# Optimization experiments

Measured on AMD Instinct MI355X. Metric: run time of the kernel, lower is better.

The kernel has to match this reference:

```python
import jax, jax.numpy as jnp
import numpy as np

N = 50000
V = 3
DIM = 128
H = 64


def setup_inputs() -> dict:
    key = jax.random.key(0)
    ks = jax.random.split(key, 8)
    x = jax.random.normal(ks[0], (N, V * DIM), dtype=jnp.float32)
    edge_index = jax.random.randint(ks[1], (2, 800000), 0, N, dtype=jnp.int64)
    Wv = jax.random.normal(ks[2], (V, DIM, H), dtype=jnp.float32) * (1.0 / np.sqrt(DIM))
    bv = jnp.zeros((V, H), dtype=jnp.float32)
    na_w = jax.random.normal(ks[3], (H, 1), dtype=jnp.float32) * (1.0 / np.sqrt(H))
    na_b = jnp.zeros((1,), dtype=jnp.float32)
    va_w1 = jax.random.normal(ks[4], (H, H // 2), dtype=jnp.float32) * (1.0 / np.sqrt(H))
    va_b1 = jnp.zeros((H // 2,), dtype=jnp.float32)
    va_w2 = jax.random.normal(ks[5], (H // 2, 1), dtype=jnp.float32) * (1.0 / np.sqrt(H // 2))
    va_b2 = jnp.zeros((1,), dtype=jnp.float32)
    cls_w = jax.random.normal(ks[6], (H, 2), dtype=jnp.float32) * (1.0 / np.sqrt(H))
    cls_b = jnp.zeros((2,), dtype=jnp.float32)
    return dict(x=x, edge_index=edge_index, Wv=Wv, bv=bv, na_w=na_w, na_b=na_b,
                va_w1=va_w1, va_b1=va_b1, va_w2=va_w2, va_b2=va_b2,
                cls_w=cls_w, cls_b=cls_b)


def reference(x, edge_index, Wv, bv, na_w, na_b, va_w1, va_b1, va_w2, va_b2, cls_w, cls_b):
    n = x.shape[0]
    # split into equal-dim views: [N, V, DIM]
    xv = x.reshape(n, V, DIM)

    # --- GCNConv (PyG defaults): linear transform, add self-loops, sym-norm aggregate, bias ---
    h = jnp.einsum('nvd,vdh->nvh', xv, Wv)  # [N, V, H]

    src = edge_index[0]
    dst = edge_index[1]
    loop = jnp.arange(n, dtype=src.dtype)
    src_full = jnp.concatenate([src, loop])
    dst_full = jnp.concatenate([dst, loop])

    ones = jnp.ones(src_full.shape[0], dtype=h.dtype)
    deg = jax.ops.segment_sum(ones, dst_full, num_segments=n)  # in-degree incl. self-loop
    dinv = jnp.where(deg > 0, 1.0 / jnp.sqrt(deg), 0.0)
    norm = dinv[src_full] * dinv[dst_full]  # [E+N]

    msgs = h[src_full] * norm[:, None, None]            # [E+N, V, H]
    agg = jax.ops.segment_sum(msgs, dst_full, num_segments=n)  # [N, V, H]
    agg = agg + bv[None, :, :]

    # ReLU
    emb = jax.nn.relu(agg)  # [N, V, H]

    # --- NodeAttentionLayer: softmax over nodes (dim=0), applied per view ---
    scores = jnp.einsum('nvh,ho->nvo', emb, na_w) + na_b  # [N, V, 1]
    att = jax.nn.softmax(scores, axis=0)
    emb_w = emb * att  # [N, V, H]

    # --- ViewAttention ---
    avg = jnp.mean(emb_w, axis=0)  # [V, H]
    vs = jnp.tanh(avg @ va_w1 + va_b1) @ va_w2 + va_b2  # [V, 1]
    vw = jax.nn.softmax(vs.T, axis=1)  # [1, V]
    fused = jnp.einsum('nvh,v->nh', emb_w, vw[0])  # [N, H]

    # --- classifier + log_softmax ---
    logits = fused @ cls_w + cls_b
    logp = jax.nn.log_softmax(logits, axis=1)
    return logp, fused, vw[0]
```

## Files before the change

### kernel.cpp

```cpp
#include <hip/hip_runtime.h>
#include <math.h>

#define NV 3
#define DIMX 128
#define HD 64
#define NVH 192
#define NBLK 256
#define NBUK 128
#define BSH 9

typedef unsigned int uint32;
typedef unsigned short ushort16;
typedef __attribute__((ext_vector_type(8))) short short8;
typedef __attribute__((ext_vector_type(4))) float f32x4;

__device__ __forceinline__ unsigned fkey(float f){
  unsigned b = __float_as_uint(f);
  return (b & 0x80000000u) ? ~b : (b | 0x80000000u);
}
__device__ __forceinline__ float unkey(unsigned k){
  return __uint_as_float((k & 0x80000000u) ? (k ^ 0x80000000u) : ~k);
}
__device__ __forceinline__ uint32 bf16rne(float f){
  uint32 u = __float_as_uint(f);
  return (u + 0x7fffu + ((u >> 16) & 1u)) >> 16;
}
__device__ __forceinline__ float bflo(uint32 p){ return __uint_as_float(p << 16); }
__device__ __forceinline__ float bfhi(uint32 p){ return __uint_as_float(p & 0xffff0000u); }
__device__ __forceinline__ float bfus(uint32 q){ return __uint_as_float(q << 16); }

__global__ __launch_bounds__(256) void k_hist(const int* __restrict__ ei, int E, int EPB,
                                              int* __restrict__ histT){
  __shared__ int sh[NBUK];
  int t = threadIdx.x, b = blockIdx.x;
  if (t < NBUK) sh[t] = 0;
  __syncthreads();
  int e0 = b*EPB, e1 = min(e0 + EPB, E);
  for (int i = e0 + t; i < e1; i += 256){
    int d = ei[E + i];
    atomicAdd(&sh[d >> BSH], 1);
  }
  __syncthreads();
  if (t < NBUK) histT[t*NBLK + b] = sh[t];
}

__global__ __launch_bounds__(1024) void k_hscan(int* __restrict__ histT){
  __shared__ int sh[1024];
  int t = threadIdx.x;
  int lo = t*32;
  int vals[32]; int s = 0;
  #pragma unroll
  for (int k = 0; k < 32; ++k){ vals[k] = histT[lo+k]; s += vals[k]; }
  sh[t] = s; __syncthreads();
  for (int ofs = 1; ofs < 1024; ofs <<= 1){
    int v = (t >= ofs) ? sh[t-ofs] : 0;
    __syncthreads();
    sh[t] += v;
    __syncthreads();
  }
  int run = sh[t] - s;
  #pragma unroll
  for (int k = 0; k < 32; ++k){ histT[lo+k] = run; run += vals[k]; }
}

__global__ __launch_bounds__(256) void k_scatter(const int* __restrict__ ei, int E, int EPB,
                                                 const int* __restrict__ ofsT, int2* __restrict__ ebuf){
  __shared__ int cur[NBUK];
  int t = threadIdx.x, b = blockIdx.x;
  if (t < NBUK) cur[t] = ofsT[t*NBLK + b];
  __syncthreads();
  int e0 = b*EPB, e1 = min(e0 + EPB, E);
  for (int i = e0 + t; i < e1; i += 256){
    int s = ei[i], d = ei[E + i];
    int pos = atomicAdd(&cur[d >> BSH], 1);
    ebuf[pos] = make_int2(s, d);
  }
}

__global__ __launch_bounds__(512) void k_csr(const int2* __restrict__ ebuf, const int* __restrict__ ofsT,
                                             int E, int N, int* __restrict__ rowstart,
                                             float* __restrict__ dinv, int* __restrict__ csr){
  __shared__ int cnt[512];
  __shared__ int pre[512];
  int t = threadIdx.x, b = blockIdx.x;
  int estart = ofsT[b*NBLK];
  int eend   = ((b+1)*NBLK < NBUK*NBLK) ? ofsT[(b+1)*NBLK] : E;
  int n0 = b << BSH;
  int nn = min(512, N - n0);
  cnt[t] = 0;
  __syncthreads();
  for (int i = estart + t; i < eend; i += 512){
    int d = ebuf[i].y;
    atomicAdd(&cnt[d - n0], 1);
  }
  __syncthreads();
  int c = cnt[t];
  pre[t] = c;
  __syncthreads();
  for (int ofs = 1; ofs < 512; ofs <<= 1){
    int v = (t >= ofs) ? pre[t-ofs] : 0;
    __syncthreads();
    pre[t] += v;
    __syncthreads();
  }
  int excl = pre[t] - c;
  if (t < nn){
    rowstart[n0 + t] = estart + excl;
    dinv[n0 + t] = rsqrtf((float)(c + 1));
  }
  if (b == gridDim.x - 1 && t == 0) rowstart[N] = E;
  cnt[t] = estart + excl;
  __syncthreads();
  for (int i = estart + t; i < eend; i += 512){
    int2 e = ebuf[i];
    int pos = atomicAdd(&cnt[e.y - n0], 1);
    csr[pos] = e.x;
  }
}

__global__ __launch_bounds__(256) void k_wpack(const float* __restrict__ Wv, uint32* __restrict__ Wb){
  int t = blockIdx.x*blockDim.x + threadIdx.x;
  if (t >= 3072) return;
  int l = t & 63, s = (t >> 6) & 3, c = (t >> 8) & 3, v = t >> 10;
  int h = c*16 + (l & 15);
  int kbase = s*32 + (l >> 4)*8;
  const float* wp = Wv + v*8192 + h;
  uint32 o[4];
  #pragma unroll
  for (int jj = 0; jj < 4; ++jj){
    uint32 lo = bf16rne(wp[(kbase + 2*jj    )*64]);
    uint32 hi = bf16rne(wp[(kbase + 2*jj + 1)*64]);
    o[jj] = lo | (hi << 16);
  }
  Wb[t*4+0] = o[0]; Wb[t*4+1] = o[1]; Wb[t*4+2] = o[2]; Wb[t*4+3] = o[3];
}

__global__ __launch_bounds__(256) void k_h(const float* __restrict__ x, const uint32* __restrict__ Wb,
                                           const float* __restrict__ dinv,
                                           uint32* __restrict__ h01, ushort16* __restrict__ h2v, int N){
  int wave = (blockIdx.x*blockDim.x + threadIdx.x) >> 6;
  int lane = threadIdx.x & 63;
  int base = wave * 32;
  if (base >= N) return;
  int jrow = lane & 15;
  int kq   = lane >> 4;

  int nl0 = base + jrow;        if (nl0 > N-1) nl0 = N-1;
  int nl1 = base + 16 + jrow;   if (nl1 > N-1) nl1 = N-1;
  const float* xr0 = x + (size_t)nl0*384 + kq*8;
  const float* xr1 = x + (size_t)nl1*384 + kq*8;
  const short8* WB = (const short8*)Wb;

  f32x4 acc0[2][4] = {};
  f32x4 acc1[2][4] = {};
  f32x4 acc2[2][4] = {};

  #pragma unroll
  for (int v = 0; v < NV; ++v){
    #pragma unroll
    for (int s = 0; s < 4; ++s){
      const float* p0 = xr0 + v*128 + s*32;
      const float* p1 = xr1 + v*128 + s*32;
      float4 f0 = *(const float4*)p0, g0 = *(const float4*)(p0+4);
      float4 f1 = *(const float4*)p1, g1 = *(const float4*)(p1+4);
      short8 a0, a1;
      a0[0]=(short)bf16rne(f0.x); a0[1]=(short)bf16rne(f0.y); a0[2]=(short)bf16rne(f0.z); a0[3]=(short)bf16rne(f0.w);
      a0[4]=(short)bf16rne(g0.x); a0[5]=(short)bf16rne(g0.y); a0[6]=(short)bf16rne(g0.z); a0[7]=(short)bf16rne(g0.w);
      a1[0]=(short)bf16rne(f1.x); a1[1]=(short)bf16rne(f1.y); a1[2]=(short)bf16rne(f1.z); a1[3]=(short)bf16rne(f1.w);
      a1[4]=(short)bf16rne(g1.x); a1[5]=(short)bf16rne(g1.y); a1[6]=(short)bf16rne(g1.z); a1[7]=(short)bf16rne(g1.w);
      #pragma unroll
      for (int c = 0; c < 4; ++c){
        short8 b = WB[(v*4 + c)*4*64 + s*64 + lane];
        if (v == 0){
          acc0[0][c] = __builtin_amdgcn_mfma_f32_16x16x32_bf16(a0, b, acc0[0][c], 0, 0, 0);
          acc0[1][c] = __builtin_amdgcn_mfma_f32_16x16x32_bf16(a1, b, acc0[1][c], 0, 0, 0);
        } else if (v == 1){
          acc1[0][c] = __builtin_amdgcn_mfma_f32_16x16x32_bf16(a0, b, acc1[0][c], 0, 0, 0);
          acc1[1][c] = __builtin_amdgcn_mfma_f32_16x16x32_bf16(a1, b, acc1[1][c], 0, 0, 0);
        } else {
          acc2[0][c] = __builtin_amdgcn_mfma_f32_16x16x32_bf16(a0, b, acc2[0][c], 0, 0, 0);
          acc2[1][c] = __builtin_amdgcn_mfma_f32_16x16x32_bf16(a1, b, acc2[1][c], 0, 0, 0);
        }
      }
    }
  }

  #pragma unroll
  for (int rt = 0; rt < 2; ++rt){
    #pragma unroll
    for (int r = 0; r < 4; ++r){
      int n = base + rt*16 + kq*4 + r;
      if (n < N){
        float dv = dinv[n];
        #pragma unroll
        for (int c = 0; c < 4; ++c){
          int h = c*16 + jrow;
          uint32 b0 = bf16rne(acc0[rt][c][r]*dv);
          uint32 b1 = bf16rne(acc1[rt][c][r]*dv);
          uint32 b2 = bf16rne(acc2[rt][c][r]*dv);
          h01[(size_t)n*64 + h] = b0 | (b1 << 16);
          h2v[(size_t)n*64 + h] = (ushort16)b2;
        }
      }
    }
  }
}

__global__ __launch_bounds__(256) void k_agg(const uint32* __restrict__ h01, const ushort16* __restrict__ h2,
                                             const int* __restrict__ rowstart, const int* __restrict__ csr,
                                             const float* __restrict__ dinv, const float* __restrict__ bv,
                                             const float* __restrict__ na_w, const float* __restrict__ na_b,
                                             ushort16* __restrict__ emb, float* __restrict__ scores, int N){
  int wid = (blockIdx.x*blockDim.x + threadIdx.x) >> 6;
  int lane = threadIdx.x & 63;
  if (wid >= N) return;
  int n = wid;
  uint32 ps = h01[(size_t)n*64 + lane];
  float a0 = bflo(ps), a1 = bfhi(ps), a2 = bfus(h2[(size_t)n*64 + lane]);
  int r0 = rowstart[n], r1 = rowstart[n+1];
  int i = r0;
  for (; i + 3 < r1; i += 4){
    int s0 = csr[i], s1 = csr[i+1], s2 = csr[i+2], s3 = csr[i+3];
    uint32 pa = h01[(size_t)s0*64 + lane];
    uint32 pb = h01[(size_t)s1*64 + lane];
    uint32 pc = h01[(size_t)s2*64 + lane];
    uint32 pd = h01[(size_t)s3*64 + lane];
    uint32 qa = h2[(size_t)s0*64 + lane];
    uint32 qb = h2[(size_t)s1*64 + lane];
    uint32 qc = h2[(size_t)s2*64 + lane];
    uint32 qd = h2[(size_t)s3*64 + lane];
    a0 += bflo(pa) + bflo(pb) + bflo(pc) + bflo(pd);
    a1 += bfhi(pa) + bfhi(pb) + bfhi(pc) + bfhi(pd);
    a2 += bfus(qa) + bfus(qb) + bfus(qc) + bfus(qd);
  }
  for (; i < r1; ++i){
    int s = csr[i];
    uint32 p = h01[(size_t)s*64 + lane];
    a0 += bflo(p); a1 += bfhi(p); a2 += bfus(h2[(size_t)s*64 + lane]);
  }
  float dv = dinv[n];
  float e0 = fmaxf(a0*dv + bv[lane],      0.f);
  float e1 = fmaxf(a1*dv + bv[64+lane],   0.f);
  float e2 = fmaxf(a2*dv + bv[128+lane],  0.f);
  ushort16* ep = emb + (size_t)n*NVH;
  ep[lane]     = (ushort16)bf16rne(e0);
  ep[64+lane]  = (ushort16)bf16rne(e1);
  ep[128+lane] = (ushort16)bf16rne(e2);
  float w = na_w[lane];
  float s0 = e0*w, s1 = e1*w, s2 = e2*w;
  #pragma unroll
  for (int ofs = 32; ofs >= 1; ofs >>= 1){
    s0 += __shfl_xor(s0, ofs);
    s1 += __shfl_xor(s1, ofs);
    s2 += __shfl_xor(s2, ofs);
  }
  if (lane == 0){
    float nb = na_b[0];
    scores[n] = s0 + nb; scores[N + n] = s1 + nb; scores[2*N + n] = s2 + nb;
  }
}

__global__ void k_max(const float* __restrict__ scores, int N, unsigned* __restrict__ maxkey){
  __shared__ float sh[256];
  int v = blockIdx.y;
  const float* sp = scores + (size_t)v*N;
  int base = blockIdx.x*2048 + threadIdx.x;
  float m = -3.0e38f;
  #pragma unroll
  for (int k = 0; k < 8; ++k){
    int i = base + k*256;
    if (i < N) m = fmaxf(m, sp[i]);
  }
  sh[threadIdx.x] = m; __syncthreads();
  for (int ofs = 128; ofs >= 1; ofs >>= 1){
    if (threadIdx.x < ofs) sh[threadIdx.x] = fmaxf(sh[threadIdx.x], sh[threadIdx.x+ofs]);
    __syncthreads();
  }
  if (threadIdx.x == 0) atomicMax(&maxkey[v], fkey(sh[0]));
}

__global__ __launch_bounds__(256) void k_wsum(const ushort16* __restrict__ emb, const float* __restrict__ scores,
                                              const unsigned* __restrict__ maxkey, float* __restrict__ wsum,
                                              float* __restrict__ sumexp, int N){
  __shared__ float shw[4][NVH];
  __shared__ float shse[4][4];
  int t = threadIdx.x;
  int lane = t & 63;
  int wv = t >> 6;
  int gw = (blockIdx.x*blockDim.x + t) >> 6;
  int nw = (gridDim.x*blockDim.x) >> 6;
  float m0 = unkey(maxkey[0]), m1 = unkey(maxkey[1]), m2 = unkey(maxkey[2]);
  float w0=0.f, w1=0.f, w2=0.f, se0=0.f, se1=0.f, se2=0.f;
  for (int n = gw; n < N; n += nw){
    const ushort16* ep = emb + (size_t)n*NVH;
    float x0 = expf(scores[n]       - m0);
    float x1 = expf(scores[N + n]   - m1);
    float x2 = expf(scores[2*N + n] - m2);
    w0 += bfus(ep[lane])*x0; w1 += bfus(ep[64+lane])*x1; w2 += bfus(ep[128+lane])*x2;
    se0 += x0; se1 += x1; se2 += x2;
  }
  shw[wv][lane]     = w0;
  shw[wv][64+lane]  = w1;
  shw[wv][128+lane] = w2;
  #pragma unroll
  for (int ofs = 32; ofs >= 1; ofs >>= 1){
    se0 += __shfl_xor(se0, ofs);
    se1 += __shfl_xor(se1, ofs);
    se2 += __shfl_xor(se2, ofs);
  }
  if (lane == 0){ shse[wv][0] = se0; shse[wv][1] = se1; shse[wv][2] = se2; }
  __syncthreads();
  if (t < NVH){
    float s = shw[0][t] + shw[1][t] + shw[2][t] + shw[3][t];
    atomicAdd(&wsum[t], s);
  } else if (t >= NVH && t < NVH+3){
    int v = t - NVH;
    float s = shse[0][v] + shse[1][v] + shse[2][v] + shse[3][v];
    atomicAdd(&sumexp[v], s);
  }
}

__global__ __launch_bounds__(64) void k_view(const float* __restrict__ wsum, const float* __restrict__ sumexp,
                                             const float* __restrict__ va_w1, const float* __restrict__ va_b1,
                                             const float* __restrict__ va_w2, const float* __restrict__ va_b2,
                                             float* __restrict__ g, float* __restrict__ out_vw, int N){
  __shared__ float avg[NV][64];
  __shared__ float z1[NV][32];
  int t = threadIdx.x;
  if (t < 64){
    for (int v = 0; v < NV; ++v) avg[v][t] = wsum[v*64+t] / (sumexp[v] * (float)N);
  }
  __syncthreads();
  if (t < 32){
    for (int v = 0; v < NV; ++v){
      float a = va_b1[t];
      for (int h = 0; h < 64; ++h) a += avg[v][h]*va_w1[h*32 + t];
      z1[v][t] = tanhf(a);
    }
  }
  __syncthreads();
  if (t == 0){
    float vs[NV];
    for (int v = 0; v < NV; ++v){
      float a = va_b2[0];
      for (int j = 0; j < 32; ++j) a += z1[v][j]*va_w2[j];
      vs[v] = a;
    }
    float m = fmaxf(vs[0], fmaxf(vs[1], vs[2]));
    float e0 = expf(vs[0]-m), e1 = expf(vs[1]-m), e2 = expf(vs[2]-m);
    float inv = 1.f/(e0+e1+e2);
    float vw0 = e0*inv, vw1 = e1*inv, vw2 = e2*inv;
    out_vw[0] = vw0; out_vw[1] = vw1; out_vw[2] = vw2;
    g[0] = vw0/sumexp[0]; g[1] = vw1/sumexp[1]; g[2] = vw2/sumexp[2];
  }
}

__global__ __launch_bounds__(256) void k_fused(const ushort16* __restrict__ emb, const float* __restrict__ scores,
                                               const unsigned* __restrict__ maxkey, const float* __restrict__ g,
                                               const float* __restrict__ cls_w, const float* __restrict__ cls_b,
                                               float* __restrict__ out, int N){
  int wid = (blockIdx.x*blockDim.x + threadIdx.x) >> 6;
  int lane = threadIdx.x & 63;
  if (wid >= N) return;
  int n = wid;
  float m0 = unkey(maxkey[0]), m1 = unkey(maxkey[1]), m2 = unkey(maxkey[2]);
  float w0 = expf(scores[n]       - m0)*g[0];
  float w1 = expf(scores[N + n]   - m1)*g[1];
  float w2 = expf(scores[2*N + n] - m2)*g[2];
  const ushort16* ep = emb + (size_t)n*NVH;
  float fu = bfus(ep[lane])*w0 + bfus(ep[64+lane])*w1 + bfus(ep[128+lane])*w2;
  out[(size_t)2*N + (size_t)n*64 + lane] = fu;
  float c0 = fu*cls_w[lane*2 + 0];
  float c1 = fu*cls_w[lane*2 + 1];
  #pragma unroll
  for (int ofs = 32; ofs >= 1; ofs >>= 1){
    c0 += __shfl_xor(c0, ofs);
    c1 += __shfl_xor(c1, ofs);
  }
  if (lane == 0){
    float l0 = c0 + cls_b[0], l1 = c1 + cls_b[1];
    float m = fmaxf(l0, l1);
    float lse = m + logf(expf(l0-m) + expf(l1-m));
    out[(size_t)n*2]     = l0 - lse;
    out[(size_t)n*2 + 1] = l1 - lse;
  }
}

extern "C" void kernel_launch(void* const* d_in, const int* in_sizes, int n_in,
                              void* d_out, int out_size, void* d_ws, size_t ws_size,
                              hipStream_t stream){
  const float* x     = (const float*)d_in[0];
  const int*   ei    = (const int*)d_in[1];
  const float* Wv    = (const float*)d_in[2];
  const float* bv    = (const float*)d_in[3];
  const float* na_w  = (const float*)d_in[4];
  const float* na_b  = (const float*)d_in[5];
  const float* va_w1 = (const float*)d_in[6];
  const float* va_b1 = (const float*)d_in[7];
  const float* va_w2 = (const float*)d_in[8];
  const float* va_b2 = (const float*)d_in[9];
  const float* cls_w = (const float*)d_in[10];
  const float* cls_b = (const float*)d_in[11];
  int N = in_sizes[0] / (NV*DIMX);
  int E = in_sizes[1] / 2;
  float* out = (float*)d_out;

  char* wptr = (char*)d_ws;
  size_t off = 0;
  auto alloc = [&](size_t bytes){ void* p = wptr + off; off += (bytes + 255) & ~255ull; return p; };
  uint32*    h01      = (uint32*)alloc((size_t)N*64*4);
  ushort16*  h2       = (ushort16*)alloc((size_t)N*64*2);
  ushort16*  emb      = (ushort16*)alloc((size_t)N*NVH*2);
  int*       csr      = (int*)alloc((size_t)E*4);
  int2*      ebuf     = (int2*)alloc((size_t)E*8);
  int*       histT    = (int*)alloc((size_t)NBUK*NBLK*4);
  int*       rowstart = (int*)alloc((size_t)(N+1)*4);
  float*     dinv     = (float*)alloc((size_t)N*4);
  float*     scores   = (float*)alloc((size_t)3*N*4);
  unsigned*  maxkey   = (unsigned*)alloc(3*4);
  float*     sumexp   = (float*)alloc(3*4);
  float*     wsum     = (float*)alloc(192*4);
  float*     g        = (float*)alloc(3*4);
  uint32*    Wb       = (uint32*)alloc(3072*16);

  hipMemsetAsync(maxkey, 0, 3*4, stream);
  hipMemsetAsync(sumexp, 0, 3*4, stream);
  hipMemsetAsync(wsum,   0, 192*4, stream);

  int EPB = (E + NBLK - 1) / NBLK;
  int nbuck = (N + 511) >> BSH;
  k_hist   <<<NBLK, 256, 0, stream>>>(ei, E, EPB, histT);
  k_hscan  <<<1, 1024, 0, stream>>>(histT);
  k_scatter<<<NBLK, 256, 0, stream>>>(ei, E, EPB, histT, ebuf);
  k_csr    <<<nbuck, 512, 0, stream>>>(ebuf, histT, E, N, rowstart, dinv, csr);
  k_wpack  <<<12, 256, 0, stream>>>(Wv, Wb);
  int waves = (N + 31) / 32;
  k_h      <<<(waves*64+255)/256, 256, 0, stream>>>(x, Wb, dinv, h01, h2, N);
  k_agg    <<<(N*64+255)/256, 256, 0, stream>>>(h01, h2, rowstart, csr, dinv, bv, na_w, na_b, emb, scores, N);
  dim3 gm((N+2047)/2048, NV);
  k_max    <<<gm, 256, 0, stream>>>(scores, N, maxkey);
  k_wsum   <<<304, 256, 0, stream>>>(emb, scores, maxkey, wsum, sumexp, N);
  k_view   <<<1, 64, 0, stream>>>(wsum, sumexp, va_w1, va_b1, va_w2, va_b2, g,
                                  out + (size_t)2*N + (size_t)N*64, N);
  k_fused  <<<(N*64+255)/256, 256, 0, stream>>>(emb, scores, maxkey, g, cls_w, cls_b, out, N);
}
```

Before: 168.2 us.

## Quantize node features to int8 with per-node scale, split aggregation per view

```diff
diff --git a/kernel.cpp b/kernel.cpp
--- a/kernel.cpp
+++ b/kernel.cpp
@@ -11,6 +11,7 @@
 
 typedef unsigned int uint32;
 typedef unsigned short ushort16;
+typedef unsigned char uchar;
 typedef __attribute__((ext_vector_type(8))) short short8;
 typedef __attribute__((ext_vector_type(4))) float f32x4;
 
@@ -25,8 +26,6 @@
   uint32 u = __float_as_uint(f);
   return (u + 0x7fffu + ((u >> 16) & 1u)) >> 16;
 }
-__device__ __forceinline__ float bflo(uint32 p){ return __uint_as_float(p << 16); }
-__device__ __forceinline__ float bfhi(uint32 p){ return __uint_as_float(p & 0xffff0000u); }
 __device__ __forceinline__ float bfus(uint32 q){ return __uint_as_float(q << 16); }
 
 __global__ __launch_bounds__(256) void k_hist(const int* __restrict__ ei, int E, int EPB,
@@ -64,7 +63,7 @@
 }
 
 __global__ __launch_bounds__(256) void k_scatter(const int* __restrict__ ei, int E, int EPB,
-                                                 const int* __restrict__ ofsT, int2* __restrict__ ebuf){
+                                                 const int* __restrict__ ofsT, uint32* __restrict__ ebuf){
   __shared__ int cur[NBUK];
   int t = threadIdx.x, b = blockIdx.x;
   if (t < NBUK) cur[t] = ofsT[t*NBLK + b];
@@ -73,11 +72,11 @@
   for (int i = e0 + t; i < e1; i += 256){
     int s = ei[i], d = ei[E + i];
     int pos = atomicAdd(&cur[d >> BSH], 1);
-    ebuf[pos] = make_int2(s, d);
-  }
-}
-
-__global__ __launch_bounds__(512) void k_csr(const int2* __restrict__ ebuf, const int* __restrict__ ofsT,
+    ebuf[pos] = ((uint32)(d & 511) << 16) | (uint32)s;
+  }
+}
+
+__global__ __launch_bounds__(512) void k_csr(const uint32* __restrict__ ebuf, const int* __restrict__ ofsT,
                                              int E, int N, int* __restrict__ rowstart,
                                              float* __restrict__ dinv, int* __restrict__ csr){
   __shared__ int cnt[512];
@@ -90,8 +89,7 @@
   cnt[t] = 0;
   __syncthreads();
   for (int i = estart + t; i < eend; i += 512){
-    int d = ebuf[i].y;
-    atomicAdd(&cnt[d - n0], 1);
+    atomicAdd(&cnt[ebuf[i] >> 16], 1);
   }
   __syncthreads();
   int c = cnt[t];
@@ -112,9 +110,9 @@
   cnt[t] = estart + excl;
   __syncthreads();
   for (int i = estart + t; i < eend; i += 512){
-    int2 e = ebuf[i];
-    int pos = atomicAdd(&cnt[e.y - n0], 1);
-    csr[pos] = e.x;
+    uint32 e = ebuf[i];
+    int pos = atomicAdd(&cnt[e >> 16], 1);
+    csr[pos] = (int)(e & 0xFFFFu);
   }
 }
 
@@ -137,7 +135,8 @@
 
 __global__ __launch_bounds__(256) void k_h(const float* __restrict__ x, const uint32* __restrict__ Wb,
                                            const float* __restrict__ dinv,
-                                           uint32* __restrict__ h01, ushort16* __restrict__ h2v, int N){
+                                           uint32* __restrict__ h80, uint32* __restrict__ h81,
+                                           uint32* __restrict__ h82, float* __restrict__ scale, int N){
   int wave = (blockIdx.x*blockDim.x + threadIdx.x) >> 6;
   int lane = threadIdx.x & 63;
   int base = wave * 32;
@@ -190,93 +189,96 @@
     #pragma unroll
     for (int r = 0; r < 4; ++r){
       int n = base + rt*16 + kq*4 + r;
+      float dv = (n < N) ? dinv[n] : 0.f;
+      float v0[4], v1[4], v2[4];
+      float m = 0.f;
+      #pragma unroll
+      for (int c = 0; c < 4; ++c){
+        v0[c] = acc0[rt][c][r]*dv;
+        v1[c] = acc1[rt][c][r]*dv;
+        v2[c] = acc2[rt][c][r]*dv;
+        m = fmaxf(m, fabsf(v0[c]));
+        m = fmaxf(m, fabsf(v1[c]));
+        m = fmaxf(m, fabsf(v2[c]));
+      }
+      #pragma unroll
+      for (int ofs = 1; ofs < 16; ofs <<= 1) m = fmaxf(m, __shfl_xor(m, ofs));
+      float inv = (m > 0.f) ? 127.0f/m : 0.f;
+      uint32 p0 = 0, p1 = 0, p2 = 0;
+      #pragma unroll
+      for (int c = 0; c < 4; ++c){
+        uint32 q0 = (uint32)(int)(v0[c]*inv + 128.5f);
+        uint32 q1 = (uint32)(int)(v1[c]*inv + 128.5f);
+        uint32 q2 = (uint32)(int)(v2[c]*inv + 128.5f);
+        p0 |= q0 << (8*c); p1 |= q1 << (8*c); p2 |= q2 << (8*c);
+      }
       if (n < N){
-        float dv = dinv[n];
-        #pragma unroll
-        for (int c = 0; c < 4; ++c){
-          int h = c*16 + jrow;
-          uint32 b0 = bf16rne(acc0[rt][c][r]*dv);
-          uint32 b1 = bf16rne(acc1[rt][c][r]*dv);
-          uint32 b2 = bf16rne(acc2[rt][c][r]*dv);
-          h01[(size_t)n*64 + h] = b0 | (b1 << 16);
-          h2v[(size_t)n*64 + h] = (ushort16)b2;
-        }
+        h80[n*16 + jrow] = p0;
+        h81[n*16 + jrow] = p1;
+        h82[n*16 + jrow] = p2;
+        if (jrow == 0) scale[n] = m * (1.0f/127.0f);
       }
     }
   }
 }
 
-__global__ __launch_bounds__(256) void k_agg(const uint32* __restrict__ h01, const ushort16* __restrict__ h2,
-                                             const int* __restrict__ rowstart, const int* __restrict__ csr,
-                                             const float* __restrict__ dinv, const float* __restrict__ bv,
-                                             const float* __restrict__ na_w, const float* __restrict__ na_b,
-                                             ushort16* __restrict__ emb, float* __restrict__ scores, int N){
-  int wid = (blockIdx.x*blockDim.x + threadIdx.x) >> 6;
-  int lane = threadIdx.x & 63;
-  if (wid >= N) return;
-  int n = wid;
-  uint32 ps = h01[(size_t)n*64 + lane];
-  float a0 = bflo(ps), a1 = bfhi(ps), a2 = bfus(h2[(size_t)n*64 + lane]);
-  int r0 = rowstart[n], r1 = rowstart[n+1];
-  int i = r0;
-  for (; i + 3 < r1; i += 4){
-    int s0 = csr[i], s1 = csr[i+1], s2 = csr[i+2], s3 = csr[i+3];
-    uint32 pa = h01[(size_t)s0*64 + lane];
-    uint32 pb = h01[(size_t)s1*64 + lane];
-    uint32 pc = h01[(size_t)s2*64 + lane];
-    uint32 pd = h01[(size_t)s3*64 + lane];
-    uint32 qa = h2[(size_t)s0*64 + lane];
-    uint32 qb = h2[(size_t)s1*64 + lane];
-    uint32 qc = h2[(size_t)s2*64 + lane];
-    uint32 qd = h2[(size_t)s3*64 + lane];
-    a0 += bflo(pa) + bflo(pb) + bflo(pc) + bflo(pd);
-    a1 += bfhi(pa) + bfhi(pb) + bfhi(pc) + bfhi(pd);
-    a2 += bfus(qa) + bfus(qb) + bfus(qc) + bfus(qd);
-  }
-  for (; i < r1; ++i){
-    int s = csr[i];
-    uint32 p = h01[(size_t)s*64 + lane];
-    a0 += bflo(p); a1 += bfhi(p); a2 += bfus(h2[(size_t)s*64 + lane]);
-  }
-  float dv = dinv[n];
-  float e0 = fmaxf(a0*dv + bv[lane],      0.f);
-  float e1 = fmaxf(a1*dv + bv[64+lane],   0.f);
-  float e2 = fmaxf(a2*dv + bv[128+lane],  0.f);
-  ushort16* ep = emb + (size_t)n*NVH;
-  ep[lane]     = (ushort16)bf16rne(e0);
-  ep[64+lane]  = (ushort16)bf16rne(e1);
-  ep[128+lane] = (ushort16)bf16rne(e2);
-  float w = na_w[lane];
-  float s0 = e0*w, s1 = e1*w, s2 = e2*w;
-  #pragma unroll
-  for (int ofs = 32; ofs >= 1; ofs >>= 1){
-    s0 += __shfl_xor(s0, ofs);
-    s1 += __shfl_xor(s1, ofs);
-    s2 += __shfl_xor(s2, ofs);
-  }
-  if (lane == 0){
-    float nb = na_b[0];
-    scores[n] = s0 + nb; scores[N + n] = s1 + nb; scores[2*N + n] = s2 + nb;
-  }
-}
-
-__global__ void k_max(const float* __restrict__ scores, int N, unsigned* __restrict__ maxkey){
-  __shared__ float sh[256];
-  int v = blockIdx.y;
-  const float* sp = scores + (size_t)v*N;
-  int base = blockIdx.x*2048 + threadIdx.x;
-  float m = -3.0e38f;
-  #pragma unroll
-  for (int k = 0; k < 8; ++k){
-    int i = base + k*256;
-    if (i < N) m = fmaxf(m, sp[i]);
-  }
-  sh[threadIdx.x] = m; __syncthreads();
-  for (int ofs = 128; ofs >= 1; ofs >>= 1){
-    if (threadIdx.x < ofs) sh[threadIdx.x] = fmaxf(sh[threadIdx.x], sh[threadIdx.x+ofs]);
-    __syncthreads();
-  }
-  if (threadIdx.x == 0) atomicMax(&maxkey[v], fkey(sh[0]));
+__global__ __launch_bounds__(256) void k_aggv(const uchar* __restrict__ h8, const float* __restrict__ scale,
+                                              const int* __restrict__ rowstart, const int* __restrict__ csr,
+                                              const float* __restrict__ dinv, const float* __restrict__ bv_v,
+                                              const float* __restrict__ na_w, const float* __restrict__ na_b,
+                                              ushort16* __restrict__ emb_v, float* __restrict__ scores_v,
+                                              unsigned* __restrict__ maxkey_v, int N){
+  __shared__ unsigned bmax;
+  int t = threadIdx.x;
+  if (t == 0) bmax = 0u;
+  __syncthreads();
+  int n = blockIdx.x*4 + (t >> 6);
+  int l = t & 63;
+  int hp = (l & 3)*16 + (l >> 2);
+  if (n < N){
+    uint32 qs = h8[(size_t)n*64 + l];
+    float scs = scale[n];
+    float a = scs * (float)qs;
+    float ssum = scs;
+    int r0 = rowstart[n], r1 = rowstart[n+1];
+    int i = r0;
+    for (; i + 3 < r1; i += 4){
+      int s0 = __builtin_nontemporal_load(&csr[i]);
+      int s1 = __builtin_nontemporal_load(&csr[i+1]);
+      int s2 = __builtin_nontemporal_load(&csr[i+2]);
+      int s3 = __builtin_nontemporal_load(&csr[i+3]);
+      uint32 q0 = h8[(size_t)s0*64 + l];
+      uint32 q1 = h8[(size_t)s1*64 + l];
+      uint32 q2 = h8[(size_t)s2*64 + l];
+      uint32 q3 = h8[(size_t)s3*64 + l];
+      float c0 = scale[s0], c1 = scale[s1], c2 = scale[s2], c3 = scale[s3];
+      a = fmaf(c0, (float)q0, a);
+      a = fmaf(c1, (float)q1, a);
+      a = fmaf(c2, (float)q2, a);
+      a = fmaf(c3, (float)q3, a);
+      ssum += c0 + c1 + c2 + c3;
+    }
+    for (; i < r1; ++i){
+      int s = __builtin_nontemporal_load(&csr[i]);
+      uint32 q = h8[(size_t)s*64 + l];
+      float sc = scale[s];
+      a = fmaf(sc, (float)q, a);
+      ssum += sc;
+    }
+    a -= 128.0f*ssum;
+    float e = fmaxf(a*dinv[n] + bv_v[hp], 0.f);
+    __builtin_nontemporal_store((ushort16)bf16rne(e), &emb_v[(size_t)n*NVH + hp]);
+    float s = e * na_w[hp];
+    #pragma unroll
+    for (int ofs = 32; ofs >= 1; ofs >>= 1) s += __shfl_xor(s, ofs);
+    if (l == 0){
+      float score = s + na_b[0];
+      scores_v[n] = score;
+      atomicMax(&bmax, fkey(score));
+    }
+  }
+  __syncthreads();
+  if (t == 0) atomicMax(maxkey_v, bmax);
 }
 
 __global__ __launch_bounds__(256) void k_wsum(const ushort16* __restrict__ emb, const float* __restrict__ scores,
@@ -408,11 +410,13 @@
   char* wptr = (char*)d_ws;
   size_t off = 0;
   auto alloc = [&](size_t bytes){ void* p = wptr + off; off += (bytes + 255) & ~255ull; return p; };
-  uint32*    h01      = (uint32*)alloc((size_t)N*64*4);
-  ushort16*  h2       = (ushort16*)alloc((size_t)N*64*2);
+  uint32*    h80      = (uint32*)alloc((size_t)N*64);
+  uint32*    h81      = (uint32*)alloc((size_t)N*64);
+  uint32*    h82      = (uint32*)alloc((size_t)N*64);
+  float*     scale    = (float*)alloc((size_t)N*4);
   ushort16*  emb      = (ushort16*)alloc((size_t)N*NVH*2);
   int*       csr      = (int*)alloc((size_t)E*4);
-  int2*      ebuf     = (int2*)alloc((size_t)E*8);
+  uint32*    ebuf     = (uint32*)alloc((size_t)E*4);
   int*       histT    = (int*)alloc((size_t)NBUK*NBLK*4);
   int*       rowstart = (int*)alloc((size_t)(N+1)*4);
   float*     dinv     = (float*)alloc((size_t)N*4);
@@ -435,10 +439,14 @@
   k_csr    <<<nbuck, 512, 0, stream>>>(ebuf, histT, E, N, rowstart, dinv, csr);
   k_wpack  <<<12, 256, 0, stream>>>(Wv, Wb);
   int waves = (N + 31) / 32;
-  k_h      <<<(waves*64+255)/256, 256, 0, stream>>>(x, Wb, dinv, h01, h2, N);
-  k_agg    <<<(N*64+255)/256, 256, 0, stream>>>(h01, h2, rowstart, csr, dinv, bv, na_w, na_b, emb, scores, N);
-  dim3 gm((N+2047)/2048, NV);
-  k_max    <<<gm, 256, 0, stream>>>(scores, N, maxkey);
+  k_h      <<<(waves*64+255)/256, 256, 0, stream>>>(x, Wb, dinv, h80, h81, h82, scale, N);
+  int gagg = (N + 3) / 4;
+  k_aggv   <<<gagg, 256, 0, stream>>>((const uchar*)h80, scale, rowstart, csr, dinv, bv,
+                                      na_w, na_b, emb,      scores,       maxkey,   N);
+  k_aggv   <<<gagg, 256, 0, stream>>>((const uchar*)h81, scale, rowstart, csr, dinv, bv + 64,
+                                      na_w, na_b, emb + 64, scores + N,   maxkey+1, N);
+  k_aggv   <<<gagg, 256, 0, stream>>>((const uchar*)h82, scale, rowstart, csr, dinv, bv + 128,
+                                      na_w, na_b, emb + 128, scores + 2*N, maxkey+2, N);
   k_wsum   <<<304, 256, 0, stream>>>(emb, scores, maxkey, wsum, sumexp, N);
   k_view   <<<1, 64, 0, stream>>>(wsum, sumexp, va_w1, va_b1, va_w2, va_b2, g,
                                   out + (size_t)2*N + (size_t)N*64, N);
```

Result: slower. 574.5 us (+241.5%).

## Quantize node features to 8-bit with per-tile scales and pack edge buffer

Applied to the files above, without the earlier changes.

```diff
diff --git a/kernel.cpp b/kernel.cpp
--- a/kernel.cpp
+++ b/kernel.cpp
@@ -11,6 +11,7 @@
 
 typedef unsigned int uint32;
 typedef unsigned short ushort16;
+typedef unsigned char uchar;
 typedef __attribute__((ext_vector_type(8))) short short8;
 typedef __attribute__((ext_vector_type(4))) float f32x4;
 
@@ -25,9 +26,14 @@
   uint32 u = __float_as_uint(f);
   return (u + 0x7fffu + ((u >> 16) & 1u)) >> 16;
 }
-__device__ __forceinline__ float bflo(uint32 p){ return __uint_as_float(p << 16); }
-__device__ __forceinline__ float bfhi(uint32 p){ return __uint_as_float(p & 0xffff0000u); }
 __device__ __forceinline__ float bfus(uint32 q){ return __uint_as_float(q << 16); }
+
+__global__ void k_zero(float* __restrict__ wsum, float* __restrict__ sumexp, unsigned* __restrict__ maxkey){
+  int t = threadIdx.x;
+  if (t < NVH) wsum[t] = 0.f;
+  else if (t < NVH+3) sumexp[t-NVH] = 0.f;
+  else if (t < NVH+6) maxkey[t-NVH-3] = 0u;
+}
 
 __global__ __launch_bounds__(256) void k_hist(const int* __restrict__ ei, int E, int EPB,
                                               int* __restrict__ histT){
@@ -64,7 +70,7 @@
 }
 
 __global__ __launch_bounds__(256) void k_scatter(const int* __restrict__ ei, int E, int EPB,
-                                                 const int* __restrict__ ofsT, int2* __restrict__ ebuf){
+                                                 const int* __restrict__ ofsT, uint32* __restrict__ ebuf){
   __shared__ int cur[NBUK];
   int t = threadIdx.x, b = blockIdx.x;
   if (t < NBUK) cur[t] = ofsT[t*NBLK + b];
@@ -73,11 +79,11 @@
   for (int i = e0 + t; i < e1; i += 256){
     int s = ei[i], d = ei[E + i];
     int pos = atomicAdd(&cur[d >> BSH], 1);
-    ebuf[pos] = make_int2(s, d);
-  }
-}
-
-__global__ __launch_bounds__(512) void k_csr(const int2* __restrict__ ebuf, const int* __restrict__ ofsT,
+    ebuf[pos] = ((uint32)(d & 511) << 16) | (uint32)s;
+  }
+}
+
+__global__ __launch_bounds__(512) void k_csr(const uint32* __restrict__ ebuf, const int* __restrict__ ofsT,
                                              int E, int N, int* __restrict__ rowstart,
                                              float* __restrict__ dinv, int* __restrict__ csr){
   __shared__ int cnt[512];
@@ -90,8 +96,7 @@
   cnt[t] = 0;
   __syncthreads();
   for (int i = estart + t; i < eend; i += 512){
-    int d = ebuf[i].y;
-    atomicAdd(&cnt[d - n0], 1);
+    atomicAdd(&cnt[ebuf[i] >> 16], 1);
   }
   __syncthreads();
   int c = cnt[t];
@@ -112,9 +117,9 @@
   cnt[t] = estart + excl;
   __syncthreads();
   for (int i = estart + t; i < eend; i += 512){
-    int2 e = ebuf[i];
-    int pos = atomicAdd(&cnt[e.y - n0], 1);
-    csr[pos] = e.x;
+    uint32 e = ebuf[i];
+    int pos = atomicAdd(&cnt[e >> 16], 1);
+    csr[pos] = (int)(e & 0xFFFFu);
   }
 }
 
@@ -137,116 +142,110 @@
 
 __global__ __launch_bounds__(256) void k_h(const float* __restrict__ x, const uint32* __restrict__ Wb,
                                            const float* __restrict__ dinv,
-                                           uint32* __restrict__ h01, ushort16* __restrict__ h2v, int N){
-  int wave = (blockIdx.x*blockDim.x + threadIdx.x) >> 6;
+                                           uint32* __restrict__ hq32, float* __restrict__ scaleV,
+                                           int N, int NT){
+  int wv = (blockIdx.x*blockDim.x + threadIdx.x) >> 6;
   int lane = threadIdx.x & 63;
-  int base = wave * 32;
-  if (base >= N) return;
+  int tile = wv / 3;
+  int v = wv - tile*3;
+  if (tile >= NT) return;
   int jrow = lane & 15;
   int kq   = lane >> 4;
-
-  int nl0 = base + jrow;        if (nl0 > N-1) nl0 = N-1;
-  int nl1 = base + 16 + jrow;   if (nl1 > N-1) nl1 = N-1;
-  const float* xr0 = x + (size_t)nl0*384 + kq*8;
-  const float* xr1 = x + (size_t)nl1*384 + kq*8;
+  int nrow = tile*16 + jrow;
+  const float* xr = x + (size_t)nrow*384 + v*128 + kq*8;
   const short8* WB = (const short8*)Wb;
 
-  f32x4 acc0[2][4] = {};
-  f32x4 acc1[2][4] = {};
-  f32x4 acc2[2][4] = {};
-
-  #pragma unroll
-  for (int v = 0; v < NV; ++v){
+  f32x4 acc[4] = {};
+  #pragma unroll
+  for (int s = 0; s < 4; ++s){
+    const float* p = xr + s*32;
+    float4 f = *(const float4*)p, g = *(const float4*)(p+4);
+    short8 a;
+    a[0]=(short)bf16rne(f.x); a[1]=(short)bf16rne(f.y); a[2]=(short)bf16rne(f.z); a[3]=(short)bf16rne(f.w);
+    a[4]=(short)bf16rne(g.x); a[5]=(short)bf16rne(g.y); a[6]=(short)bf16rne(g.z); a[7]=(short)bf16rne(g.w);
     #pragma unroll
-    for (int s = 0; s < 4; ++s){
-      const float* p0 = xr0 + v*128 + s*32;
-      const float* p1 = xr1 + v*128 + s*32;
-      float4 f0 = *(const float4*)p0, g0 = *(const float4*)(p0+4);
-      float4 f1 = *(const float4*)p1, g1 = *(const float4*)(p1+4);
-      short8 a0, a1;
-      a0[0]=(short)bf16rne(f0.x); a0[1]=(short)bf16rne(f0.y); a0[2]=(short)bf16rne(f0.z); a0[3]=(short)bf16rne(f0.w);
-      a0[4]=(short)bf16rne(g0.x); a0[5]=(short)bf16rne(g0.y); a0[6]=(short)bf16rne(g0.z); a0[7]=(short)bf16rne(g0.w);
-      a1[0]=(short)bf16rne(f1.x); a1[1]=(short)bf16rne(f1.y); a1[2]=(short)bf16rne(f1.z); a1[3]=(short)bf16rne(f1.w);
-      a1[4]=(short)bf16rne(g1.x); a1[5]=(short)bf16rne(g1.y); a1[6]=(short)bf16rne(g1.z); a1[7]=(short)bf16rne(g1.w);
-      #pragma unroll
-      for (int c = 0; c < 4; ++c){
-        short8 b = WB[(v*4 + c)*4*64 + s*64 + lane];
-        if (v == 0){
-          acc0[0][c] = __builtin_amdgcn_mfma_f32_16x16x32_bf16(a0, b, acc0[0][c], 0, 0, 0);
-          acc0[1][c] = __builtin_amdgcn_mfma_f32_16x16x32_bf16(a1, b, acc0[1][c], 0, 0, 0);
-        } else if (v == 1){
-          acc1[0][c] = __builtin_amdgcn_mfma_f32_16x16x32_bf16(a0, b, acc1[0][c], 0, 0, 0);
-          acc1[1][c] = __builtin_amdgcn_mfma_f32_16x16x32_bf16(a1, b, acc1[1][c], 0, 0, 0);
-        } else {
-          acc2[0][c] = __builtin_amdgcn_mfma_f32_16x16x32_bf16(a0, b, acc2[0][c], 0, 0, 0);
-          acc2[1][c] = __builtin_amdgcn_mfma_f32_16x16x32_bf16(a1, b, acc2[1][c], 0, 0, 0);
-        }
-      }
-    }
-  }
-
-  #pragma unroll
-  for (int rt = 0; rt < 2; ++rt){
+    for (int c = 0; c < 4; ++c){
+      short8 b = WB[(v*4 + c)*256 + s*64 + lane];
+      acc[c] = __builtin_amdgcn_mfma_f32_16x16x32_bf16(a, b, acc[c], 0, 0, 0);
+    }
+  }
+
+  float vv[4][4];
+  float mx = 0.f;
+  #pragma unroll
+  for (int r = 0; r < 4; ++r){
+    int n = tile*16 + kq*4 + r;
+    float dv = dinv[n];
     #pragma unroll
-    for (int r = 0; r < 4; ++r){
-      int n = base + rt*16 + kq*4 + r;
-      if (n < N){
-        float dv = dinv[n];
-        #pragma unroll
-        for (int c = 0; c < 4; ++c){
-          int h = c*16 + jrow;
-          uint32 b0 = bf16rne(acc0[rt][c][r]*dv);
-          uint32 b1 = bf16rne(acc1[rt][c][r]*dv);
-          uint32 b2 = bf16rne(acc2[rt][c][r]*dv);
-          h01[(size_t)n*64 + h] = b0 | (b1 << 16);
-          h2v[(size_t)n*64 + h] = (ushort16)b2;
-        }
-      }
-    }
-  }
-}
-
-__global__ __launch_bounds__(256) void k_agg(const uint32* __restrict__ h01, const ushort16* __restrict__ h2,
-                                             const int* __restrict__ rowstart, const int* __restrict__ csr,
-                                             const float* __restrict__ dinv, const float* __restrict__ bv,
-                                             const float* __restrict__ na_w, const float* __restrict__ na_b,
-                                             ushort16* __restrict__ emb, float* __restrict__ scores, int N){
+    for (int c = 0; c < 4; ++c){
+      float t = acc[c][r]*dv;
+      vv[c][r] = t;
+      mx = fmaxf(mx, fabsf(t));
+    }
+  }
+  #pragma unroll
+  for (int ofs = 1; ofs < 64; ofs <<= 1) mx = fmaxf(mx, __shfl_xor(mx, ofs));
+  float inv = (mx > 0.f) ? 127.0f/mx : 0.f;
+  #pragma unroll
+  for (int r = 0; r < 4; ++r){
+    int n = tile*16 + kq*4 + r;
+    uint32 w = 0;
+    #pragma unroll
+    for (int c = 0; c < 4; ++c){
+      uint32 q = (uint32)(int)(vv[c][r]*inv + 128.5f);
+      w |= q << (8*c);
+    }
+    hq32[(size_t)n*48 + v*16 + jrow] = w;
+  }
+  if (lane == 0) scaleV[v*NT + tile] = mx * (1.0f/127.0f);
+}
+
+__global__ __launch_bounds__(256) void k_aggv(const uchar* __restrict__ hq, const float* __restrict__ scaleV,
+                                              const int* __restrict__ rowstart, const int* __restrict__ csr,
+                                              const float* __restrict__ dinv, const float* __restrict__ bv,
+                                              const float* __restrict__ na_w, const float* __restrict__ na_b,
+                                              ushort16* __restrict__ emb, float* __restrict__ scores,
+                                              int N, int NT){
   int wid = (blockIdx.x*blockDim.x + threadIdx.x) >> 6;
   int lane = threadIdx.x & 63;
   if (wid >= N) return;
   int n = wid;
-  uint32 ps = h01[(size_t)n*64 + lane];
-  float a0 = bflo(ps), a1 = bfhi(ps), a2 = bfus(h2[(size_t)n*64 + lane]);
+  int hp = (lane & 3)*16 + (lane >> 2);
+  const uchar* hb = hq + (size_t)n*192;
+  float q0 = (float)hb[lane], q1 = (float)hb[64+lane], q2 = (float)hb[128+lane];
+  int grp = n >> 4;
+  float c0 = scaleV[grp], c1 = scaleV[NT+grp], c2 = scaleV[2*NT+grp];
+  float a0 = c0*q0, a1 = c1*q1, a2 = c2*q2;
+  float ss0 = c0, ss1 = c1, ss2 = c2;
   int r0 = rowstart[n], r1 = rowstart[n+1];
-  int i = r0;
-  for (; i + 3 < r1; i += 4){
-    int s0 = csr[i], s1 = csr[i+1], s2 = csr[i+2], s3 = csr[i+3];
-    uint32 pa = h01[(size_t)s0*64 + lane];
-    uint32 pb = h01[(size_t)s1*64 + lane];
-    uint32 pc = h01[(size_t)s2*64 + lane];
-    uint32 pd = h01[(size_t)s3*64 + lane];
-    uint32 qa = h2[(size_t)s0*64 + lane];
-    uint32 qb = h2[(size_t)s1*64 + lane];
-    uint32 qc = h2[(size_t)s2*64 + lane];
-    uint32 qd = h2[(size_t)s3*64 + lane];
-    a0 += bflo(pa) + bflo(pb) + bflo(pc) + bflo(pd);
-    a1 += bfhi(pa) + bfhi(pb) + bfhi(pc) + bfhi(pd);
-    a2 += bfus(qa) + bfus(qb) + bfus(qc) + bfus(qd);
-  }
-  for (; i < r1; ++i){
-    int s = csr[i];
-    uint32 p = h01[(size_t)s*64 + lane];
-    a0 += bflo(p); a1 += bfhi(p); a2 += bfus(h2[(size_t)s*64 + lane]);
-  }
+  for (int base = r0; base < r1; base += 64){
+    int m = r1 - base; if (m > 64) m = 64;
+    int sv = (lane < m) ? __builtin_nontemporal_load(&csr[base + lane]) : 0;
+    for (int i = 0; i < m; ++i){
+      int s = __shfl(sv, i);
+      const uchar* hs = hq + (size_t)s*192;
+      float b0 = (float)hs[lane];
+      float b1 = (float)hs[64+lane];
+      float b2 = (float)hs[128+lane];
+      int g2 = s >> 4;
+      float d0 = scaleV[g2], d1 = scaleV[NT+g2], d2 = scaleV[2*NT+g2];
+      a0 = fmaf(d0, b0, a0); ss0 += d0;
+      a1 = fmaf(d1, b1, a1); ss1 += d1;
+      a2 = fmaf(d2, b2, a2); ss2 += d2;
+    }
+  }
+  a0 -= 128.0f*ss0;
+  a1 -= 128.0f*ss1;
+  a2 -= 128.0f*ss2;
   float dv = dinv[n];
-  float e0 = fmaxf(a0*dv + bv[lane],      0.f);
-  float e1 = fmaxf(a1*dv + bv[64+lane],   0.f);
-  float e2 = fmaxf(a2*dv + bv[128+lane],  0.f);
+  float e0 = fmaxf(a0*dv + bv[hp],      0.f);
+  float e1 = fmaxf(a1*dv + bv[64+hp],   0.f);
+  float e2 = fmaxf(a2*dv + bv[128+hp],  0.f);
   ushort16* ep = emb + (size_t)n*NVH;
-  ep[lane]     = (ushort16)bf16rne(e0);
-  ep[64+lane]  = (ushort16)bf16rne(e1);
-  ep[128+lane] = (ushort16)bf16rne(e2);
-  float w = na_w[lane];
+  __builtin_nontemporal_store((ushort16)bf16rne(e0), &ep[hp]);
+  __builtin_nontemporal_store((ushort16)bf16rne(e1), &ep[64+hp]);
+  __builtin_nontemporal_store((ushort16)bf16rne(e2), &ep[128+hp]);
+  float w = na_w[hp];
   float s0 = e0*w, s1 = e1*w, s2 = e2*w;
   #pragma unroll
   for (int ofs = 32; ofs >= 1; ofs >>= 1){
@@ -404,15 +403,16 @@
   int N = in_sizes[0] / (NV*DIMX);
   int E = in_sizes[1] / 2;
   float* out = (float*)d_out;
+  int NT = (N + 15) / 16;
 
   char* wptr = (char*)d_ws;
   size_t off = 0;
   auto alloc = [&](size_t bytes){ void* p = wptr + off; off += (bytes + 255) & ~255ull; return p; };
-  uint32*    h01      = (uint32*)alloc((size_t)N*64*4);
-  ushort16*  h2       = (ushort16*)alloc((size_t)N*64*2);
+  uint32*    hq       = (uint32*)alloc((size_t)N*48*4);
+  float*     scaleV   = (float*)alloc((size_t)3*NT*4);
   ushort16*  emb      = (ushort16*)alloc((size_t)N*NVH*2);
   int*       csr      = (int*)alloc((size_t)E*4);
-  int2*      ebuf     = (int2*)alloc((size_t)E*8);
+  uint32*    ebuf     = (uint32*)alloc((size_t)E*4);
   int*       histT    = (int*)alloc((size_t)NBUK*NBLK*4);
   int*       rowstart = (int*)alloc((size_t)(N+1)*4);
   float*     dinv     = (float*)alloc((size_t)N*4);
@@ -423,20 +423,18 @@
   float*     g        = (float*)alloc(3*4);
   uint32*    Wb       = (uint32*)alloc(3072*16);
 
-  hipMemsetAsync(maxkey, 0, 3*4, stream);
-  hipMemsetAsync(sumexp, 0, 3*4, stream);
-  hipMemsetAsync(wsum,   0, 192*4, stream);
-
   int EPB = (E + NBLK - 1) / NBLK;
   int nbuck = (N + 511) >> BSH;
+  k_zero   <<<1, 256, 0, stream>>>(wsum, sumexp, maxkey);
   k_hist   <<<NBLK, 256, 0, stream>>>(ei, E, EPB, histT);
   k_hscan  <<<1, 1024, 0, stream>>>(histT);
   k_scatter<<<NBLK, 256, 0, stream>>>(ei, E, EPB, histT, ebuf);
   k_csr    <<<nbuck, 512, 0, stream>>>(ebuf, histT, E, N, rowstart, dinv, csr);
   k_wpack  <<<12, 256, 0, stream>>>(Wv, Wb);
-  int waves = (N + 31) / 32;
-  k_h      <<<(waves*64+255)/256, 256, 0, stream>>>(x, Wb, dinv, h01, h2, N);
-  k_agg    <<<(N*64+255)/256, 256, 0, stream>>>(h01, h2, rowstart, csr, dinv, bv, na_w, na_b, emb, scores, N);
+  int hwaves = NT*3;
+  k_h      <<<(hwaves*64+255)/256, 256, 0, stream>>>(x, Wb, dinv, hq, scaleV, N, NT);
+  k_aggv   <<<(N*64+255)/256, 256, 0, stream>>>((const uchar*)hq, scaleV, rowstart, csr, dinv, bv,
+                                                na_w, na_b, emb, scores, N, NT);
   dim3 gm((N+2047)/2048, NV);
   k_max    <<<gm, 256, 0, stream>>>(scores, N, maxkey);
   k_wsum   <<<304, 256, 0, stream>>>(emb, scores, maxkey, wsum, sumexp, N);
```

Result: slower. 184.5 us (+9.7%).
